# Performance work log

Measured on AMD Instinct MI355X. Metric: run time of the kernel, lower is better.

Reference implementation:

```python
import jax, jax.numpy as jnp
import numpy as np

D_IN = 512
D = 1024      # new_embed_dim
H = 16        # num_heads
HD = D // H   # head_dim


def setup_inputs() -> dict:
    key = jax.random.key(0)
    ks = jax.random.split(key, 16)
    g = lambda k, shape, fan: jax.random.normal(k, shape, jnp.float32) / np.sqrt(fan)
    return {
        "x1": jax.random.normal(ks[0], (16, 1, D_IN), jnp.float32),
        "x2": jax.random.normal(ks[1], (16, 4096, D_IN), jnp.float32),
        "x3": jax.random.normal(ks[2], (16, 4096, D_IN), jnp.float32),
        # embedding1 (for x1) and embedding2 (used for BOTH x2 and x3, per source)
        "We1": g(ks[3], (D_IN, D), D_IN), "be1": jnp.zeros((D,), jnp.float32),
        "We2": g(ks[4], (D_IN, D), D_IN), "be2": jnp.zeros((D,), jnp.float32),
        "Wq": g(ks[5], (D, D), D), "bq": jnp.zeros((D,), jnp.float32),
        "Wk": g(ks[6], (D, D), D), "bk": jnp.zeros((D,), jnp.float32),
        "Wv": g(ks[7], (D, D), D), "bv": jnp.zeros((D,), jnp.float32),
        "Wo": g(ks[8], (D, D), D), "bo": jnp.zeros((D,), jnp.float32),
    }


def reference(x1, x2, x3, We1, be1, We2, be2, Wq, bq, Wk, bk, Wv, bv, Wo, bo):
    B = x1.shape[0]
    # embeddings (x3 intentionally uses embedding2's weights, matching source)
    x1e = x1 @ We1 + be1                      # [B,1,D]
    x2e = x2 @ We2 + be2                      # [B,S,D]
    x3e = x3 @ We2 + be2                      # [B,S,D]
    q = (x1e @ Wq + bq).reshape(B, -1, H, HD).transpose(0, 2, 1, 3)  # [B,H,1,HD]
    k = (x2e @ Wk + bk).reshape(B, -1, H, HD).transpose(0, 2, 1, 3)  # [B,H,S,HD]
    v = (x3e @ Wv + bv).reshape(B, -1, H, HD).transpose(0, 2, 1, 3)  # [B,H,S,HD]
    scale = jnp.asarray(np.sqrt(HD), q.dtype)
    attn = jax.nn.softmax(jnp.einsum("bhqd,bhkd->bhqk", q, k) / scale, axis=-1)
    # dropout is identity at inference (keras training=False default)
    av = jnp.einsum("bhqk,bhkd->bhqd", attn, v)          # [B,H,1,HD]
    av = av.transpose(0, 2, 1, 3).reshape(B, -1, D)      # [B,1,D]
    out = av @ Wo + bo                                   # [B,1,D]
    return jnp.squeeze(out, axis=1)                      # [B,D]
```

## Files before the change

### kernel.cpp

```cpp
#include <hip/hip_runtime.h>


#define DIN 512
#define DD  1024
#define NH  16
#define HD  64
#define BB  16
#define SS  4096

__device__ __forceinline__ int wave_id() {
    return __builtin_amdgcn_readfirstlane((int)(threadIdx.x >> 6));
}

__device__ __forceinline__ void tile_transpose(const float* __restrict__ in,
                                               float* __restrict__ out,
                                               int R, int C, int rblk, int cblk) {
    __shared__ float tl[32][33];
    const int tx = threadIdx.x & 31, ty = threadIdx.x >> 5;
    const int c0 = cblk * 32, r0 = rblk * 32;
#pragma unroll
    for (int k = 0; k < 4; ++k)
        tl[ty + k * 8][tx] = in[(size_t)(r0 + ty + k * 8) * C + c0 + tx];
    __syncthreads();
#pragma unroll
    for (int k = 0; k < 4; ++k)
        out[(size_t)(c0 + ty + k * 8) * R + r0 + tx] = tl[tx][ty + k * 8];
}

__global__ __launch_bounds__(256) void k_prep(const float* __restrict__ We2,
                                              const float* __restrict__ Wk,
                                              const float* __restrict__ be1,
                                              const float* __restrict__ bq,
                                              const float* __restrict__ bv,
                                              const float* __restrict__ bo,
                                              float* __restrict__ We2t,
                                              float* __restrict__ WkT,
                                              float* __restrict__ x1e,
                                              float* __restrict__ qb,
                                              float* __restrict__ av,
                                              float* __restrict__ out) {
    const int bx = blockIdx.x;
    if (bx < 512) {
        tile_transpose(We2, We2t, DIN, DD, bx >> 5, bx & 31);
    } else if (bx < 1536) {
        const int lb = bx - 512;
        tile_transpose(Wk, WkT, DD, DD, lb >> 5, lb & 31);
    } else {
        const int b = bx - 1536;
#pragma unroll
        for (int k = 0; k < 4; ++k) {
            const int c = k * 256 + threadIdx.x;
            x1e[(size_t)b * DD + c] = be1[c];
            qb[(size_t)b * DD + c]  = bq[c];
            av[(size_t)b * DD + c]  = bv[c];
            out[(size_t)b * DD + c] = bo[c];
        }
    }
}

template <int K, int N, int KS, bool HASB>
__global__ __launch_bounds__(256) void k_bmv2(const float* __restrict__ in,
                                              const float* __restrict__ W,
                                              const float* __restrict__ bias,
                                              float* __restrict__ out) {
    const int l = threadIdx.x & 63;
    const int c = blockIdx.x * 64 + l;
    const int wv = wave_id();
    constexpr int KCH = K / KS;
    constexpr int SUB = KCH / 4;
    const float* inb = in + (size_t)blockIdx.y * 16 * K;
    float acc[16];
#pragma unroll
    for (int r = 0; r < 16; ++r) acc[r] = 0.f;
    const int i0 = blockIdx.z * KCH + wv * SUB;
#pragma unroll 4
    for (int i = i0; i < i0 + SUB; ++i) {
        const float wval = W[(size_t)i * N + c];
#pragma unroll
        for (int r = 0; r < 16; ++r) acc[r] += inb[(size_t)r * K + i] * wval;
    }
    __shared__ float red[4][16][64];
#pragma unroll
    for (int r = 0; r < 16; ++r) red[wv][r][l] = acc[r];
    __syncthreads();
#pragma unroll
    for (int k = 0; k < 4; ++k) {
        const int r = wv + k * 4;
        float v = red[0][r][l] + red[1][r][l] + red[2][r][l] + red[3][r][l];
        float* dst = out + ((size_t)blockIdx.y * 16 + r) * N + c;
        if (KS == 1) {
            if (HASB) v += bias[c];
            *dst = v;
        } else {
            atomicAdd(dst, v);
        }
    }
}

__global__ __launch_bounds__(256) void k_u2(const float* __restrict__ q,
                                            const float* __restrict__ WkT,
                                            float* __restrict__ u) {
    const int h = blockIdx.y;
    const int l = threadIdx.x & 63;
    const int c = blockIdx.x * 64 + l;
    const int wv = wave_id();
    float acc[16];
#pragma unroll
    for (int bb = 0; bb < 16; ++bb) acc[bb] = 0.f;
#pragma unroll 4
    for (int dk = 0; dk < 16; ++dk) {
        const int d = wv * 16 + dk;
        const float wval = WkT[(size_t)(h * HD + d) * DD + c];
#pragma unroll
        for (int bb = 0; bb < 16; ++bb)
            acc[bb] += q[(size_t)bb * DD + h * HD + d] * wval;
    }
    __shared__ float red[4][16][64];
#pragma unroll
    for (int bb = 0; bb < 16; ++bb) red[wv][bb][l] = acc[bb];
    __syncthreads();
#pragma unroll
    for (int k = 0; k < 4; ++k) {
        const int bb = wv + k * 4;
        float v = red[0][bb][l] + red[1][bb][l] + red[2][bb][l] + red[3][bb][l];
        u[((size_t)bb * NH + h) * DD + c] = v;
    }
}

__global__ __launch_bounds__(256) void k_scores(const float* __restrict__ x2,
                                                const float* __restrict__ w,
                                                float* __restrict__ sc) {
    __shared__ float4 tile[64 * 33];
    const int b = blockIdx.y;
    const int s0 = blockIdx.x * 64;
    const int l = threadIdx.x & 63;
    const int h0 = wave_id() * 4;
    const float4* x2f = (const float4*)x2 + ((size_t)b * SS + s0) * (DIN / 4);
    const float4* wp = (const float4*)(w + ((size_t)b * NH + h0) * DIN);
    float a0 = 0.f, a1 = 0.f, a2 = 0.f, a3 = 0.f;
    for (int kt = 0; kt < 4; ++kt) {
        __syncthreads();
#pragma unroll
        for (int k = 0; k < 8; ++k) {
            const int idx = threadIdx.x + k * 256;
            const int row = idx >> 5, c4 = idx & 31;
            tile[row * 33 + c4] = x2f[row * (DIN / 4) + kt * 32 + c4];
        }
        __syncthreads();
#pragma unroll 8
        for (int c4 = 0; c4 < 32; ++c4) {
            const float4 x = tile[l * 33 + c4];
            const float4 q0 = wp[kt * 32 + c4];
            const float4 q1 = wp[128 + kt * 32 + c4];
            const float4 q2 = wp[256 + kt * 32 + c4];
            const float4 q3 = wp[384 + kt * 32 + c4];
            a0 += x.x * q0.x + x.y * q0.y + x.z * q0.z + x.w * q0.w;
            a1 += x.x * q1.x + x.y * q1.y + x.z * q1.z + x.w * q1.w;
            a2 += x.x * q2.x + x.y * q2.y + x.z * q2.z + x.w * q2.w;
            a3 += x.x * q3.x + x.y * q3.y + x.z * q3.z + x.w * q3.w;
        }
    }
    const size_t base = ((size_t)b * NH + h0) * SS + s0 + l;
    sc[base + 0 * SS] = a0;
    sc[base + 1 * SS] = a1;
    sc[base + 2 * SS] = a2;
    sc[base + 3 * SS] = a3;
}

__global__ __launch_bounds__(256) void k_softmax(float* __restrict__ sc) {
    float4* row = (float4*)(sc + (size_t)blockIdx.x * SS);
    float4 v[4];
    float m = -1e30f;
#pragma unroll
    for (int j = 0; j < 4; ++j) {
        v[j] = row[threadIdx.x + j * 256];
        m = fmaxf(m, fmaxf(fmaxf(v[j].x, v[j].y), fmaxf(v[j].z, v[j].w)));
    }
    __shared__ float red[256];
    red[threadIdx.x] = m;
    __syncthreads();
    for (int s = 128; s > 0; s >>= 1) {
        if (threadIdx.x < (unsigned)s)
            red[threadIdx.x] = fmaxf(red[threadIdx.x], red[threadIdx.x + s]);
        __syncthreads();
    }
    m = red[0];
    __syncthreads();
    float sum = 0.f;
#pragma unroll
    for (int j = 0; j < 4; ++j) {
        v[j].x = expf((v[j].x - m) * 0.125f);
        v[j].y = expf((v[j].y - m) * 0.125f);
        v[j].z = expf((v[j].z - m) * 0.125f);
        v[j].w = expf((v[j].w - m) * 0.125f);
        sum += v[j].x + v[j].y + v[j].z + v[j].w;
    }
    red[threadIdx.x] = sum;
    __syncthreads();
    for (int s = 128; s > 0; s >>= 1) {
        if (threadIdx.x < (unsigned)s) red[threadIdx.x] += red[threadIdx.x + s];
        __syncthreads();
    }
    const float inv = 1.f / red[0];
#pragma unroll
    for (int j = 0; j < 4; ++j) {
        v[j].x *= inv; v[j].y *= inv; v[j].z *= inv; v[j].w *= inv;
        row[threadIdx.x + j * 256] = v[j];
    }
}

__global__ __launch_bounds__(256) void k_gpart(const float* __restrict__ x3,
                                               const float* __restrict__ a,
                                               float* __restrict__ gp,
                                               int schunk, int nch) {
    const int b = blockIdx.y, ch = blockIdx.x;
    const int wv = wave_id();
    const int l = threadIdx.x & 63;
    const int sub = schunk >> 2;
    const int sbeg = ch * schunk + wv * sub;
    const float* ar = a + (size_t)b * NH * SS;
    float acc[16][8];
#pragma unroll
    for (int h = 0; h < 16; ++h)
#pragma unroll
        for (int j = 0; j < 8; ++j) acc[h][j] = 0.f;

#pragma unroll 2
    for (int s = sbeg; s < sbeg + sub; ++s) {
        const float4* xr = (const float4*)(x3 + ((size_t)b * SS + s) * DIN);
        const float4 xa = xr[l];
        const float4 xb = xr[l + 64];
        const float xv[8] = {xa.x, xa.y, xa.z, xa.w, xb.x, xb.y, xb.z, xb.w};
#pragma unroll
        for (int h = 0; h < 16; ++h) {
            const float wh = ar[h * SS + s];
#pragma unroll
            for (int j = 0; j < 8; ++j) acc[h][j] += wh * xv[j];
        }
    }

    __shared__ float red[4][2048];
    for (int hg = 0; hg < 4; ++hg) {
        __syncthreads();
#pragma unroll
        for (int hh = 0; hh < 4; ++hh) {
            float* dst = &red[wv][hh * 512];
            const int hs = hg * 4 + hh;
            *(float4*)(dst + l * 4) =
                make_float4(acc[hs][0], acc[hs][1], acc[hs][2], acc[hs][3]);
            *(float4*)(dst + 256 + l * 4) =
                make_float4(acc[hs][4], acc[hs][5], acc[hs][6], acc[hs][7]);
        }
        __syncthreads();
        const int idx = threadIdx.x * 8;
        float o[8];
#pragma unroll
        for (int j = 0; j < 8; ++j)
            o[j] = red[0][idx + j] + red[1][idx + j] + red[2][idx + j] + red[3][idx + j];
        const int hh = idx >> 9;
        const int i = idx & 511;
        float* dst = gp + (((size_t)(b * nch + ch) * NH) + hg * 4 + hh) * DIN + i;
        *(float4*)dst = make_float4(o[0], o[1], o[2], o[3]);
        *(float4*)(dst + 4) = make_float4(o[4], o[5], o[6], o[7]);
    }
}

__global__ __launch_bounds__(256) void k_greduce(const float* __restrict__ gp, int nch,
                                                 float* __restrict__ g) {
    const int pair = blockIdx.x;
    const int b = pair >> 4, h = pair & 15;
#pragma unroll
    for (int kk = 0; kk < 2; ++kk) {
        const int i = kk * 256 + threadIdx.x;
        float acc = 0.f;
        for (int ch = 0; ch < nch; ++ch)
            acc += gp[((size_t)(b * nch + ch) * NH + h) * DIN + i];
        g[(size_t)pair * DIN + i] = acc;
    }
}

__global__ __launch_bounds__(256) void k_av_at(const float* __restrict__ G2,
                                               const float* __restrict__ Wv,
                                               float* __restrict__ av) {
    const int h = blockIdx.x;
    const int l = threadIdx.x & 63;
    const int wv = wave_id();
    const int c0 = blockIdx.y * 128 + wv * 32;
    float acc[16];
#pragma unroll
    for (int bb = 0; bb < 16; ++bb) acc[bb] = 0.f;
#pragma unroll 4
    for (int c = c0; c < c0 + 32; ++c) {
        const float wval = Wv[(size_t)c * DD + h * HD + l];
#pragma unroll
        for (int bb = 0; bb < 16; ++bb)
            acc[bb] += G2[((size_t)bb * NH + h) * DD + c] * wval;
    }
    __shared__ float red[4][16][64];
#pragma unroll
    for (int bb = 0; bb < 16; ++bb) red[wv][bb][l] = acc[bb];
    __syncthreads();
#pragma unroll
    for (int k = 0; k < 4; ++k) {
        const int bb = wv + k * 4;
        float v = red[0][bb][l] + red[1][bb][l] + red[2][bb][l] + red[3][bb][l];
        atomicAdd(&av[(size_t)bb * DD + h * HD + l], v);
    }
}

extern "C" void kernel_launch(void* const* d_in, const int* in_sizes, int n_in,
                              void* d_out, int out_size, void* d_ws, size_t ws_size,
                              hipStream_t stream) {
    const float* x1  = (const float*)d_in[0];
    const float* x2  = (const float*)d_in[1];
    const float* x3  = (const float*)d_in[2];
    const float* We1 = (const float*)d_in[3];
    const float* be1 = (const float*)d_in[4];
    const float* We2 = (const float*)d_in[5];
    const float* be2 = (const float*)d_in[6];
    const float* Wq  = (const float*)d_in[7];
    const float* bq  = (const float*)d_in[8];
    const float* Wk  = (const float*)d_in[9];
    const float* bk  = (const float*)d_in[10];
    const float* Wv  = (const float*)d_in[11];
    const float* bv  = (const float*)d_in[12];
    const float* Wo  = (const float*)d_in[13];
    const float* bo  = (const float*)d_in[14];
    (void)bk;
    float* out = (float*)d_out;

    char* ws = (char*)d_ws;
    size_t off = 0;
    auto alloc = [&](size_t bytes) -> void* {
        void* p = ws + off;
        off = (off + bytes + 255) & ~(size_t)255;
        return p;
    };
    float* We2t = (float*)alloc((size_t)DD * DIN * 4);
    float* WkT  = (float*)alloc((size_t)DD * DD * 4);
    float* x1e  = (float*)alloc((size_t)BB * DD * 4);
    float* qb   = (float*)alloc((size_t)BB * DD * 4);
    float* u    = (float*)alloc((size_t)BB * NH * DD * 4);
    float* wv_  = (float*)alloc((size_t)BB * NH * DIN * 4);
    float* sc   = (float*)alloc((size_t)BB * NH * SS * 4);
    float* g    = (float*)alloc((size_t)BB * NH * DIN * 4);
    float* G2   = (float*)alloc((size_t)BB * NH * DD * 4);
    float* av   = (float*)alloc((size_t)BB * DD * 4);

    const size_t per_chunk = (size_t)BB * NH * DIN * 4;
    int nch = 32;
    while (nch > 8 && off + (size_t)nch * per_chunk > ws_size) nch >>= 1;
    float* gp = (float*)alloc((size_t)nch * per_chunk);
    const int schunk = SS / nch;

    k_prep<<<1552, 256, 0, stream>>>(We2, Wk, be1, bq, bv, bo,
                                     We2t, WkT, x1e, qb, av, out);
    k_bmv2<DIN, DD, 8, false><<<dim3(DD / 64, 1, 8), 256, 0, stream>>>(x1, We1, nullptr, x1e);
    k_bmv2<DD, DD, 8, false><<<dim3(DD / 64, 1, 8), 256, 0, stream>>>(x1e, Wq, nullptr, qb);
    k_u2<<<dim3(DD / 64, NH), 256, 0, stream>>>(qb, WkT, u);
    k_bmv2<DD, DIN, 1, false><<<dim3(DIN / 64, BB * NH / 16, 1), 256, 0, stream>>>(u, We2t, nullptr, wv_);
    k_scores<<<dim3(SS / 64, BB), 256, 0, stream>>>(x2, wv_, sc);
    k_softmax<<<BB * NH, 256, 0, stream>>>(sc);
    k_gpart<<<dim3(nch, BB), 256, 0, stream>>>(x3, sc, gp, schunk, nch);
    k_greduce<<<BB * NH, 256, 0, stream>>>(gp, nch, g);
    k_bmv2<DIN, DD, 1, true><<<dim3(DD / 64, BB * NH / 16, 1), 256, 0, stream>>>(g, We2, be2, G2);
    k_av_at<<<dim3(NH, 8), 256, 0, stream>>>(G2, Wv, av);
    k_bmv2<DD, DD, 8, false><<<dim3(DD / 64, 1, 8), 256, 0, stream>>>(av, Wo, nullptr, out);
}
```

Before: 465.8 us.

## Fuse scores, softmax and value accumulation into one online-softmax attention kernel

New measurement: 449.0 us. -3.6%, faster.

```diff
diff --git a/kernel.cpp b/kernel.cpp
--- a/kernel.cpp
+++ b/kernel.cpp
@@ -7,6 +7,7 @@
 #define HD  64
 #define BB  16
 #define SS  4096
+#define NCH 32
 
 __device__ __forceinline__ int wave_id() {
     return __builtin_amdgcn_readfirstlane((int)(threadIdx.x >> 6));
@@ -127,125 +128,117 @@
     }
 }
 
-__global__ __launch_bounds__(256) void k_scores(const float* __restrict__ x2,
-                                                const float* __restrict__ w,
-                                                float* __restrict__ sc) {
-    __shared__ float4 tile[64 * 33];
-    const int b = blockIdx.y;
-    const int s0 = blockIdx.x * 64;
+__global__ __launch_bounds__(256) void k_attn(const float* __restrict__ x2,
+                                              const float* __restrict__ x3,
+                                              const float* __restrict__ w,
+                                              float* __restrict__ gp,
+                                              float* __restrict__ mls) {
+    __shared__ __align__(16) char smem[64 * 33 * 16 + 16 * 64 * 4];
+    float4* tile = (float4*)smem;
+    float*  scb  = (float*)(smem + 64 * 33 * 16);
+    float*  red  = (float*)smem;
+    __shared__ float sm[4][16], sl[4][16];
+
+    const int b = blockIdx.y, ch = blockIdx.x;
     const int l = threadIdx.x & 63;
-    const int h0 = wave_id() * 4;
-    const float4* x2f = (const float4*)x2 + ((size_t)b * SS + s0) * (DIN / 4);
+    const int wv = wave_id();
+    const int h0 = wv * 4;
     const float4* wp = (const float4*)(w + ((size_t)b * NH + h0) * DIN);
-    float a0 = 0.f, a1 = 0.f, a2 = 0.f, a3 = 0.f;
-    for (int kt = 0; kt < 4; ++kt) {
+
+    float m[16], lsum[16], acc[16][8];
+#pragma unroll
+    for (int h = 0; h < 16; ++h) {
+        m[h] = -1e30f; lsum[h] = 0.f;
+#pragma unroll
+        for (int j = 0; j < 8; ++j) acc[h][j] = 0.f;
+    }
+
+    for (int t = 0; t < 2; ++t) {
+        const int s0 = ch * 128 + t * 64;
+        const float4* x2f = (const float4*)x2 + ((size_t)b * SS + s0) * (DIN / 4);
+        float a0 = 0.f, a1 = 0.f, a2 = 0.f, a3 = 0.f;
+        for (int kt = 0; kt < 4; ++kt) {
+            __syncthreads();
+#pragma unroll
+            for (int k = 0; k < 8; ++k) {
+                const int idx = threadIdx.x + k * 256;
+                const int row = idx >> 5, c4 = idx & 31;
+                tile[row * 33 + c4] = x2f[row * (DIN / 4) + kt * 32 + c4];
+            }
+            __syncthreads();
+#pragma unroll 8
+            for (int c4 = 0; c4 < 32; ++c4) {
+                const float4 x = tile[l * 33 + c4];
+                const float4 q0 = wp[kt * 32 + c4];
+                const float4 q1 = wp[128 + kt * 32 + c4];
+                const float4 q2 = wp[256 + kt * 32 + c4];
+                const float4 q3 = wp[384 + kt * 32 + c4];
+                a0 += x.x * q0.x + x.y * q0.y + x.z * q0.z + x.w * q0.w;
+                a1 += x.x * q1.x + x.y * q1.y + x.z * q1.z + x.w * q1.w;
+                a2 += x.x * q2.x + x.y * q2.y + x.z * q2.z + x.w * q2.w;
+                a3 += x.x * q3.x + x.y * q3.y + x.z * q3.z + x.w * q3.w;
+            }
+        }
+        scb[(h0 + 0) * 64 + l] = a0;
+        scb[(h0 + 1) * 64 + l] = a1;
+        scb[(h0 + 2) * 64 + l] = a2;
+        scb[(h0 + 3) * 64 + l] = a3;
         __syncthreads();
-#pragma unroll
-        for (int k = 0; k < 8; ++k) {
-            const int idx = threadIdx.x + k * 256;
-            const int row = idx >> 5, c4 = idx & 31;
-            tile[row * 33 + c4] = x2f[row * (DIN / 4) + kt * 32 + c4];
-        }
-        __syncthreads();
-#pragma unroll 8
-        for (int c4 = 0; c4 < 32; ++c4) {
-            const float4 x = tile[l * 33 + c4];
-            const float4 q0 = wp[kt * 32 + c4];
-            const float4 q1 = wp[128 + kt * 32 + c4];
-            const float4 q2 = wp[256 + kt * 32 + c4];
-            const float4 q3 = wp[384 + kt * 32 + c4];
-            a0 += x.x * q0.x + x.y * q0.y + x.z * q0.z + x.w * q0.w;
-            a1 += x.x * q1.x + x.y * q1.y + x.z * q1.z + x.w * q1.w;
-            a2 += x.x * q2.x + x.y * q2.y + x.z * q2.z + x.w * q2.w;
-            a3 += x.x * q3.x + x.y * q3.y + x.z * q3.z + x.w * q3.w;
-        }
-    }
-    const size_t base = ((size_t)b * NH + h0) * SS + s0 + l;
-    sc[base + 0 * SS] = a0;
-    sc[base + 1 * SS] = a1;
-    sc[base + 2 * SS] = a2;
-    sc[base + 3 * SS] = a3;
-}
-
-__global__ __launch_bounds__(256) void k_softmax(float* __restrict__ sc) {
-    float4* row = (float4*)(sc + (size_t)blockIdx.x * SS);
-    float4 v[4];
-    float m = -1e30f;
-#pragma unroll
-    for (int j = 0; j < 4; ++j) {
-        v[j] = row[threadIdx.x + j * 256];
-        m = fmaxf(m, fmaxf(fmaxf(v[j].x, v[j].y), fmaxf(v[j].z, v[j].w)));
-    }
-    __shared__ float red[256];
-    red[threadIdx.x] = m;
-    __syncthreads();
-    for (int s = 128; s > 0; s >>= 1) {
-        if (threadIdx.x < (unsigned)s)
-            red[threadIdx.x] = fmaxf(red[threadIdx.x], red[threadIdx.x + s]);
-        __syncthreads();
-    }
-    m = red[0];
-    __syncthreads();
-    float sum = 0.f;
-#pragma unroll
-    for (int j = 0; j < 4; ++j) {
-        v[j].x = expf((v[j].x - m) * 0.125f);
-        v[j].y = expf((v[j].y - m) * 0.125f);
-        v[j].z = expf((v[j].z - m) * 0.125f);
-        v[j].w = expf((v[j].w - m) * 0.125f);
-        sum += v[j].x + v[j].y + v[j].z + v[j].w;
-    }
-    red[threadIdx.x] = sum;
-    __syncthreads();
-    for (int s = 128; s > 0; s >>= 1) {
-        if (threadIdx.x < (unsigned)s) red[threadIdx.x] += red[threadIdx.x + s];
-        __syncthreads();
-    }
-    const float inv = 1.f / red[0];
-#pragma unroll
-    for (int j = 0; j < 4; ++j) {
-        v[j].x *= inv; v[j].y *= inv; v[j].z *= inv; v[j].w *= inv;
-        row[threadIdx.x + j * 256] = v[j];
-    }
-}
-
-__global__ __launch_bounds__(256) void k_gpart(const float* __restrict__ x3,
-                                               const float* __restrict__ a,
-                                               float* __restrict__ gp,
-                                               int schunk, int nch) {
-    const int b = blockIdx.y, ch = blockIdx.x;
-    const int wv = wave_id();
-    const int l = threadIdx.x & 63;
-    const int sub = schunk >> 2;
-    const int sbeg = ch * schunk + wv * sub;
-    const float* ar = a + (size_t)b * NH * SS;
-    float acc[16][8];
-#pragma unroll
-    for (int h = 0; h < 16; ++h)
-#pragma unroll
-        for (int j = 0; j < 8; ++j) acc[h][j] = 0.f;
-
-#pragma unroll 2
-    for (int s = sbeg; s < sbeg + sub; ++s) {
-        const float4* xr = (const float4*)(x3 + ((size_t)b * SS + s) * DIN);
-        const float4 xa = xr[l];
-        const float4 xb = xr[l + 64];
-        const float xv[8] = {xa.x, xa.y, xa.z, xa.w, xb.x, xb.y, xb.z, xb.w};
+
+        const int sq = wv * 16;
+        float tm[16];
 #pragma unroll
         for (int h = 0; h < 16; ++h) {
-            const float wh = ar[h * SS + s];
-#pragma unroll
-            for (int j = 0; j < 8; ++j) acc[h][j] += wh * xv[j];
-        }
-    }
-
-    __shared__ float red[4][2048];
+            float mm = -1e30f;
+#pragma unroll
+            for (int j = 0; j < 16; ++j) mm = fmaxf(mm, scb[h * 64 + sq + j]);
+            tm[h] = mm * 0.125f;
+        }
+#pragma unroll
+        for (int h = 0; h < 16; ++h) {
+            const float mn = fmaxf(m[h], tm[h]);
+            const float f = __expf(m[h] - mn);
+            m[h] = mn; lsum[h] *= f;
+#pragma unroll
+            for (int j = 0; j < 8; ++j) acc[h][j] *= f;
+        }
+        for (int j = 0; j < 16; ++j) {
+            const int s = s0 + sq + j;
+            const float4* xr = (const float4*)(x3 + ((size_t)b * SS + s) * DIN);
+            const float4 xa = xr[l];
+            const float4 xb = xr[l + 64];
+            const float xv[8] = {xa.x, xa.y, xa.z, xa.w, xb.x, xb.y, xb.z, xb.w};
+#pragma unroll
+            for (int h = 0; h < 16; ++h) {
+                const float e = __expf(scb[h * 64 + sq + j] * 0.125f - m[h]);
+                lsum[h] += e;
+#pragma unroll
+                for (int jj = 0; jj < 8; ++jj) acc[h][jj] += e * xv[jj];
+            }
+        }
+    }
+
+#pragma unroll
+    for (int h = 0; h < 16; ++h) sm[wv][h] = m[h];
+    __syncthreads();
+#pragma unroll
+    for (int h = 0; h < 16; ++h) {
+        const float bmh = fmaxf(fmaxf(sm[0][h], sm[1][h]), fmaxf(sm[2][h], sm[3][h]));
+        const float f = __expf(m[h] - bmh);
+        lsum[h] *= f;
+#pragma unroll
+        for (int j = 0; j < 8; ++j) acc[h][j] *= f;
+    }
+#pragma unroll
+    for (int h = 0; h < 16; ++h) sl[wv][h] = lsum[h];
+
+#pragma unroll
     for (int hg = 0; hg < 4; ++hg) {
         __syncthreads();
 #pragma unroll
         for (int hh = 0; hh < 4; ++hh) {
-            float* dst = &red[wv][hh * 512];
             const int hs = hg * 4 + hh;
+            float* dst = &red[wv * 2048 + hh * 512];
             *(float4*)(dst + l * 4) =
                 make_float4(acc[hs][0], acc[hs][1], acc[hs][2], acc[hs][3]);
             *(float4*)(dst + 256 + l * 4) =
@@ -253,29 +246,51 @@
         }
         __syncthreads();
         const int idx = threadIdx.x * 8;
-        float o[8];
-#pragma unroll
-        for (int j = 0; j < 8; ++j)
-            o[j] = red[0][idx + j] + red[1][idx + j] + red[2][idx + j] + red[3][idx + j];
         const int hh = idx >> 9;
         const int i = idx & 511;
-        float* dst = gp + (((size_t)(b * nch + ch) * NH) + hg * 4 + hh) * DIN + i;
-        *(float4*)dst = make_float4(o[0], o[1], o[2], o[3]);
-        *(float4*)(dst + 4) = make_float4(o[4], o[5], o[6], o[7]);
-    }
-}
-
-__global__ __launch_bounds__(256) void k_greduce(const float* __restrict__ gp, int nch,
-                                                 float* __restrict__ g) {
+        float o[8];
+#pragma unroll
+        for (int j = 0; j < 8; ++j)
+            o[j] = red[0 * 2048 + idx + j] + red[1 * 2048 + idx + j] +
+                   red[2 * 2048 + idx + j] + red[3 * 2048 + idx + j];
+        float* dstg = gp + (((size_t)(b * NCH + ch) * NH) + hg * 4 + hh) * DIN + i;
+        *(float4*)dstg = make_float4(o[0], o[1], o[2], o[3]);
+        *(float4*)(dstg + 4) = make_float4(o[4], o[5], o[6], o[7]);
+    }
+    if (threadIdx.x < 16) {
+        const int h = threadIdx.x;
+        const float bmh = fmaxf(fmaxf(sm[0][h], sm[1][h]), fmaxf(sm[2][h], sm[3][h]));
+        const float L = sl[0][h] + sl[1][h] + sl[2][h] + sl[3][h];
+        float* dst = mls + (((size_t)b * NCH + ch) * NH + h) * 2;
+        dst[0] = bmh;
+        dst[1] = L;
+    }
+}
+
+__global__ __launch_bounds__(256) void k_greduce2(const float* __restrict__ gp,
+                                                  const float* __restrict__ mls,
+                                                  float* __restrict__ g) {
     const int pair = blockIdx.x;
     const int b = pair >> 4, h = pair & 15;
+    float M = -1e30f;
+    for (int ch = 0; ch < NCH; ++ch)
+        M = fmaxf(M, mls[(((size_t)b * NCH + ch) * NH + h) * 2]);
+    float fch[NCH];
+    float L = 0.f;
+    for (int ch = 0; ch < NCH; ++ch) {
+        const float* p = mls + (((size_t)b * NCH + ch) * NH + h) * 2;
+        const float f = __expf(p[0] - M);
+        fch[ch] = f;
+        L += f * p[1];
+    }
+    const float invL = 1.f / L;
 #pragma unroll
     for (int kk = 0; kk < 2; ++kk) {
         const int i = kk * 256 + threadIdx.x;
         float acc = 0.f;
-        for (int ch = 0; ch < nch; ++ch)
-            acc += gp[((size_t)(b * nch + ch) * NH + h) * DIN + i];
-        g[(size_t)pair * DIN + i] = acc;
+        for (int ch = 0; ch < NCH; ++ch)
+            acc += fch[ch] * gp[((size_t)(b * NCH + ch) * NH + h) * DIN + i];
+        g[(size_t)pair * DIN + i] = acc * invL;
     }
 }
 
@@ -342,16 +357,11 @@
     float* qb   = (float*)alloc((size_t)BB * DD * 4);
     float* u    = (float*)alloc((size_t)BB * NH * DD * 4);
     float* wv_  = (float*)alloc((size_t)BB * NH * DIN * 4);
-    float* sc   = (float*)alloc((size_t)BB * NH * SS * 4);
     float* g    = (float*)alloc((size_t)BB * NH * DIN * 4);
     float* G2   = (float*)alloc((size_t)BB * NH * DD * 4);
     float* av   = (float*)alloc((size_t)BB * DD * 4);
-
-    const size_t per_chunk = (size_t)BB * NH * DIN * 4;
-    int nch = 32;
-    while (nch > 8 && off + (size_t)nch * per_chunk > ws_size) nch >>= 1;
-    float* gp = (float*)alloc((size_t)nch * per_chunk);
-    const int schunk = SS / nch;
+    float* gp   = (float*)alloc((size_t)BB * NCH * NH * DIN * 4);
+    float* mls  = (float*)alloc((size_t)BB * NCH * NH * 2 * 4);
 
     k_prep<<<1552, 256, 0, stream>>>(We2, Wk, be1, bq, bv, bo,
                                      We2t, WkT, x1e, qb, av, out);
@@ -359,10 +369,8 @@
     k_bmv2<DD, DD, 8, false><<<dim3(DD / 64, 1, 8), 256, 0, stream>>>(x1e, Wq, nullptr, qb);
     k_u2<<<dim3(DD / 64, NH), 256, 0, stream>>>(qb, WkT, u);
     k_bmv2<DD, DIN, 1, false><<<dim3(DIN / 64, BB * NH / 16, 1), 256, 0, stream>>>(u, We2t, nullptr, wv_);
-    k_scores<<<dim3(SS / 64, BB), 256, 0, stream>>>(x2, wv_, sc);
-    k_softmax<<<BB * NH, 256, 0, stream>>>(sc);
-    k_gpart<<<dim3(nch, BB), 256, 0, stream>>>(x3, sc, gp, schunk, nch);
-    k_greduce<<<BB * NH, 256, 0, stream>>>(gp, nch, g);
+    k_attn<<<dim3(NCH, BB), 256, 0, stream>>>(x2, x3, wv_, gp, mls);
+    k_greduce2<<<BB * NH, 256, 0, stream>>>(gp, mls, g);
     k_bmv2<DIN, DD, 1, true><<<dim3(DD / 64, BB * NH / 16, 1), 256, 0, stream>>>(g, We2, be2, G2);
     k_av_at<<<dim3(NH, 8), 256, 0, stream>>>(G2, Wv, av);
     k_bmv2<DD, DD, 8, false><<<dim3(DD / 64, 1, 8), 256, 0, stream>>>(av, Wo, nullptr, out);
```
